# Kernel optimization log

Hardware: AMD Instinct MI355X
Metric: run time of the kernel (lower is better)

The kernel has to match this reference:

```python
import jax, jax.numpy as jnp
import numpy as np

N, H, HD = 512, 8, 128          # n_nodes, n_heads, h feature dim
M0, M1 = 256, 256               # mlp_units
NORM_CONST = 1.0


def setup_inputs() -> dict:
    key = jax.random.key(0)
    ks = jax.random.split(key, 16)
    def w(k, i, o, scale=1.0):
        return jax.random.normal(k, (i, o), jnp.float32) * (scale / np.sqrt(i))
    F = HD + H * H               # h_concat dim = 128 + 64 = 192
    EIN = H + 2 * F              # edge MLP input dim = 8 + 384 = 392
    return {
        "x": jax.random.normal(ks[0], (N, H, 3), jnp.float32),
        "h": jax.random.normal(ks[1], (N, HD), jnp.float32),
        # phi_e: MLP([256,256], silu, activate_final=True)
        "We0": w(ks[2], EIN, M0), "be0": jnp.zeros((M0,), jnp.float32),
        "We1": w(ks[3], M0, M1), "be1": jnp.zeros((M1,), jnp.float32),
        # phi_inf: Linear(1) + sigmoid
        "Winf": w(ks[4], M1, 1), "binf": jnp.zeros((1,), jnp.float32),
        # phi_x: MLP([256,256], silu, activate_final=True) -> Linear(n_heads) (variance-scaled small init)
        "Wx0": w(ks[5], M1, M0), "bx0": jnp.zeros((M0,), jnp.float32),
        "Wx1": w(ks[6], M0, M1), "bx1": jnp.zeros((M1,), jnp.float32),
        "Wxo": w(ks[7], M1, H, scale=0.03), "bxo": jnp.zeros((H,), jnp.float32),
        # phi_h: MLP([256,256], silu, activate_final=False)... note haiku MLP applies
        # activation between layers; final Linear(h_dim) appended in forward.
        "Wh0": w(ks[8], M1 + HD, M0), "bh0": jnp.zeros((M0,), jnp.float32),
        "Wh1": w(ks[9], M0, M1), "bh1": jnp.zeros((M1,), jnp.float32),
        "Who": w(ks[10], M1, HD), "bho": jnp.zeros((HD,), jnp.float32),
    }


def _forward(x, h, We0, be0, We1, be1, Winf, binf, Wx0, bx0, Wx1, bx1,
             Wxo, bxo, Wh0, bh0, Wh1, bh1, Who, bho):
    n, nh = x.shape[0], x.shape[1]
    silu = jax.nn.silu
    off = 1.0 - jnp.eye(n, dtype=x.dtype)                  # off-diagonal node mask
    # per-node head-pair squared distances -> [N, H*H] (diag naturally 0)
    dh = x[:, :, None, :] - x[:, None, :, :]               # [N,H,H,3]
    sqh = jnp.sum(dh * dh, axis=-1).reshape(n, nh * nh)
    hc = jnp.concatenate([h, sqh], axis=-1)                # [N, F]
    # all-pairs node diffs per head: dn[i,j,h] = x[j,h] - x[i,h]
    dn = x[None] - x[:, None]                              # [N,N,H,3]
    sqn = jnp.sum(dn * dn, axis=-1)                        # [N,N,H]
    F = hc.shape[-1]
    hc_j = jnp.broadcast_to(hc[None], (n, n, F))           # receiver-side: hc[j]
    hc_i = jnp.broadcast_to(hc[:, None], (n, n, F))        # sender-side: hc[i]
    edge_in = jnp.concatenate([sqn, hc_j, hc_i], axis=-1)  # [N,N,H+2F]
    # phi_e (activate_final=True), zero self-edges
    m = silu(silu(edge_in @ We0 + be0) @ We1 + be1) * off[:, :, None]
    # gate + message aggregation
    e = jax.nn.sigmoid(m @ Winf + binf)[..., 0] * off      # [N,N]
    m_i = jnp.einsum('ijd,ij->id', m, e)                   # [N,M1]
    # phi_x multi-head coordinate weights (tanh=False), zero self-edges
    px = (silu(silu(m @ Wx0 + bx0) @ Wx1 + bx1) @ Wxo + bxo) * off[:, :, None]
    # normalize_by_x_norm=True path
    norm = jnp.sqrt(sqn + 1e-8) + NORM_CONST               # [N,N,H]
    ndiff = (dn / norm[..., None]) * off[:, :, None, None]
    shift = jnp.einsum('ijhd,ijh->ihd', ndiff, px) / (n - 1)  # agg='mean'
    x_new = x + shift
    # phi_h with residual
    ph_in = jnp.concatenate([m_i, h], axis=-1)
    h_new = h + silu(silu(ph_in @ Wh0 + bh0) @ Wh1 + bh1) @ Who + bho
    return x_new, h_new


def reference(x, h, We0, be0, We1, be1, Winf, binf, Wx0, bx0, Wx1, bx1,
              Wxo, bxo, Wh0, bh0, Wh1, bh1, Who, bho):
    return _forward(x, h, We0, be0, We1, be1, Winf, binf, Wx0, bx0, Wx1, bx1,
                    Wxo, bxo, Wh0, bh0, Wh1, bh1, Who, bho)
```

## Files before the change

kernel.cpp:

```cpp
#include <hip/hip_runtime.h>
#include <math.h>

#define N_NODES 512
#define NH 8
#define HD 128
#define M 256
#define JTILE 64

typedef __bf16 v8bf __attribute__((ext_vector_type(8)));
typedef float f32x4 __attribute__((ext_vector_type(4)));
typedef unsigned uint2v __attribute__((ext_vector_type(2)));

__device__ __forceinline__ float silu_f(float v) {
  return v * __builtin_amdgcn_rcpf(1.f + __expf(-v));
}
__device__ __forceinline__ float sigmoid_f(float v) {
  return __builtin_amdgcn_rcpf(1.f + __expf(-v));
}
__device__ __forceinline__ unsigned short f2bf(float f) {
  unsigned u = __float_as_uint(f);
  u += 0x7fffu + ((u >> 16) & 1u);
  return (unsigned short)(u >> 16);
}
__device__ __forceinline__ float bf2f_lo(unsigned u) {
  return __uint_as_float(u << 16);
}
__device__ __forceinline__ float bf2f_hi(unsigned u) {
  return __uint_as_float(u & 0xffff0000u);
}
__device__ __forceinline__ unsigned cvt_pk_bf16(float lo, float hi) {
  unsigned r;
  asm("v_cvt_pk_bf16_f32 %0, %1, %2" : "=v"(r) : "v"(lo), "v"(hi));
  return r;
}

__global__ __launch_bounds__(256) void k_pre(
    const float* __restrict__ x, const float* __restrict__ h,
    const float* __restrict__ We0, const float* __restrict__ be0,
    const float* __restrict__ We1, const float* __restrict__ Wx0,
    const float* __restrict__ Wx1, const float* __restrict__ Wxo,
    unsigned short* __restrict__ wsB,
    float* __restrict__ P, float* __restrict__ Q,
    float* __restrict__ mi, float* __restrict__ shift)
{
  const int t = threadIdx.x;
  if (blockIdx.x < 816) {
    const int gid = blockIdx.x * 256 + t;
    if (gid >= 208896) return;
    float val;
    int dst;
    if (gid < 196608) {
      const int layer = gid >> 16, e = gid & 65535;
      const int k = e >> 8, n = e & 255;
      const float* W = (layer == 0) ? We1 : (layer == 1) ? Wx0 : Wx1;
      val = W[e];
      const int kt = k >> 5, w = k & 31, quad = w >> 3, j = w & 7;
      const int nt = n >> 4, lnib = n & 15;
      dst = layer * 65536 + ((kt * 16 + nt) * 64 + quad * 16 + lnib) * 8 + j;
    } else if (gid < 198656) {
      const int e = gid - 196608;
      val = Wxo[e];
      const int k = e >> 3, col = e & 7;
      const int kt = k >> 5, w = k & 31, quad = w >> 3, j = w & 7;
      dst = 196608 + (kt * 64 + quad * 16 + col) * 8 + j;
    } else if (gid < 200704) {
      const int e = gid - 198656;
      val = 0.f;
      const int k = e >> 3, col = e & 7;
      const int kt = k >> 5, w = k & 31, quad = w >> 3, j = w & 7;
      dst = 196608 + (kt * 64 + quad * 16 + col + 8) * 8 + j;
    } else if (gid < 202752) {
      const int e = gid - 200704;
      val = We0[e];
      const int j = e >> 8, n = e & 255, nt = n >> 4, lnib = n & 15;
      dst = 200704 + (nt * 64 + lnib) * 8 + j;
    } else {
      const int e = gid - 202752;
      val = 0.f;
      const int q = 1 + (e >> 11), rem = e & 2047;
      const int j = rem & 7, lnib = (rem >> 3) & 15, nt = rem >> 7;
      dst = 200704 + (nt * 64 + q * 16 + lnib) * 8 + j;
    }
    wsB[dst] = f2bf(val);
    return;
  }
  const int i = blockIdx.x - 816;
  __shared__ float s_x[24];
  __shared__ float s_hc[192];
  mi[i * M + t] = 0.f;
  if (t < 24) { shift[i * 24 + t] = 0.f; s_x[t] = x[i * 24 + t]; }
  __syncthreads();
  if (t < HD) {
    s_hc[t] = h[i * HD + t];
  } else if (t < 192) {
    const int p = t - HD, a = p >> 3, b = p & 7;
    float s = 0.f;
#pragma unroll
    for (int d = 0; d < 3; ++d) {
      const float dx = s_x[a * 3 + d] - s_x[b * 3 + d];
      s = fmaf(dx, dx, s);
    }
    s_hc[t] = s;
  }
  __syncthreads();
  float p = 0.f, q = 0.f;
  for (int k = 0; k < 192; ++k) {
    const float hv = s_hc[k];
    p = fmaf(hv, We0[(8 + k) * M + t], p);
    q = fmaf(hv, We0[(200 + k) * M + t], q);
  }
  P[i * M + t] = p;
  Q[i * M + t] = q + be0[t];
}

__global__ __launch_bounds__(256, 3) void k_edge(
    const float* __restrict__ x,
    const float* __restrict__ P, const float* __restrict__ Q,
    const float* __restrict__ be1,
    const float* __restrict__ Winf, const float* __restrict__ binf,
    const float* __restrict__ bx0, const float* __restrict__ bx1,
    const float* __restrict__ bxo,
    const unsigned short* __restrict__ wsB,
    float* __restrict__ mi_acc, float* __restrict__ shift_acc)
{
  const int i  = blockIdx.x;
  const int j0 = blockIdx.y * JTILE;
  const int t  = threadIdx.x;
  const int lane = t & 63, wq = t >> 6;
  const int lnib = lane & 15, quad = lane >> 4;
  const int cb = wq * 64;

  __shared__ __align__(16) unsigned short a_act[32 * 512];
  __shared__ __align__(16) float s_sqn[JTILE][8];
  __shared__ __align__(16) unsigned short s_sqnb[JTILE][8];
  __shared__ float s_red[JTILE][4];
  __shared__ float s_e[JTILE];

  f32x4 acc[4][4];

  auto store_frag = [&](int ct, int et, unsigned w0, unsigned w1) {
    const int tile = et * 8 + 2 * wq + (ct >> 1);
    const int qp   = (ct & 1) * 2 + (quad >> 1);
    const int sidx = (tile * 64 + qp * 16 + lnib) * 8 + (quad & 1) * 4;
    *(uint2v*)&a_act[sidx] = (uint2v){w0, w1};
  };

  auto run_gemm = [&](const unsigned short* __restrict__ Bg) {
#pragma unroll
    for (int kt = 0; kt < 8; ++kt) {
      v8bf wf[4], af[4];
#pragma unroll
      for (int ct = 0; ct < 4; ++ct)
        wf[ct] = *(const v8bf*)&Bg[((kt * 16 + wq * 4 + ct) * 64 + lane) * 8];
#pragma unroll
      for (int et = 0; et < 4; ++et)
        af[et] = *(const v8bf*)&a_act[((et * 8 + kt) * 64 + lane) * 8];
#pragma unroll
      for (int ct = 0; ct < 4; ++ct)
#pragma unroll
        for (int et = 0; et < 4; ++et)
          acc[ct][et] = __builtin_amdgcn_mfma_f32_16x16x32_bf16(wf[ct], af[et], acc[ct][et], 0, 0, 0);
    }
  };

#pragma unroll
  for (int kk = 0; kk < 2; ++kk) {
    const int idx = kk * 256 + t;
    const int r = idx >> 3, hh = idx & 7;
    const int j = j0 + r;
    float s = 0.f;
#pragma unroll
    for (int d = 0; d < 3; ++d) {
      const float dx = x[j * 24 + hh * 3 + d] - x[i * 24 + hh * 3 + d];
      s = fmaf(dx, dx, s);
    }
    s_sqn[r][hh] = s;
    s_sqnb[r][hh] = f2bf(s);
  }
  const float binf0 = binf[0];
  __syncthreads();

  {
#pragma unroll
    for (int ct = 0; ct < 4; ++ct)
#pragma unroll
      for (int et = 0; et < 4; ++et)
        acc[ct][et] = *(const f32x4*)&P[(j0 + et * 16 + lnib) * M + cb + ct * 16 + quad * 4];
    const unsigned short* W0 = wsB + 200704;
    v8bf wf[4], af[4];
#pragma unroll
    for (int ct = 0; ct < 4; ++ct)
      wf[ct] = *(const v8bf*)&W0[((wq * 4 + ct) * 64 + lane) * 8];
#pragma unroll
    for (int et = 0; et < 4; ++et)
      af[et] = *(const v8bf*)&s_sqnb[et * 16 + lnib][0];
#pragma unroll
    for (int ct = 0; ct < 4; ++ct)
#pragma unroll
      for (int et = 0; et < 4; ++et)
        acc[ct][et] = __builtin_amdgcn_mfma_f32_16x16x32_bf16(wf[ct], af[et], acc[ct][et], 0, 0, 0);
#pragma unroll
    for (int ct = 0; ct < 4; ++ct) {
      const f32x4 qv = *(const f32x4*)&Q[i * M + cb + ct * 16 + quad * 4];
#pragma unroll
      for (int et = 0; et < 4; ++et) {
        const unsigned w0 = cvt_pk_bf16(silu_f(acc[ct][et][0] + qv[0]),
                                        silu_f(acc[ct][et][1] + qv[1]));
        const unsigned w1 = cvt_pk_bf16(silu_f(acc[ct][et][2] + qv[2]),
                                        silu_f(acc[ct][et][3] + qv[3]));
        store_frag(ct, et, w0, w1);
      }
    }
  }

#pragma unroll
  for (int ct = 0; ct < 4; ++ct) {
    const f32x4 b = *(const f32x4*)&be1[cb + ct * 16 + quad * 4];
#pragma unroll
    for (int et = 0; et < 4; ++et) acc[ct][et] = b;
  }
  __syncthreads();
  run_gemm(wsB);
  __syncthreads();

  unsigned mw[4][4][2];
  {
    float ge[4] = {0.f, 0.f, 0.f, 0.f};
#pragma unroll
    for (int ct = 0; ct < 4; ++ct) {
      const f32x4 wv = *(const f32x4*)&Winf[cb + ct * 16 + quad * 4];
#pragma unroll
      for (int et = 0; et < 4; ++et) {
        const int row = et * 16 + lnib;
        const bool dz = (j0 + row == i);
        const float v0 = dz ? 0.f : silu_f(acc[ct][et][0]);
        const float v1 = dz ? 0.f : silu_f(acc[ct][et][1]);
        const float v2 = dz ? 0.f : silu_f(acc[ct][et][2]);
        const float v3 = dz ? 0.f : silu_f(acc[ct][et][3]);
        ge[et] = fmaf(v0, wv[0], ge[et]);
        ge[et] = fmaf(v1, wv[1], ge[et]);
        ge[et] = fmaf(v2, wv[2], ge[et]);
        ge[et] = fmaf(v3, wv[3], ge[et]);
        const unsigned w0 = cvt_pk_bf16(v0, v1);
        const unsigned w1 = cvt_pk_bf16(v2, v3);
        mw[ct][et][0] = w0; mw[ct][et][1] = w1;
        store_frag(ct, et, w0, w1);
      }
    }
#pragma unroll
    for (int et = 0; et < 4; ++et) {
      float g = ge[et];
      g += __shfl_xor(g, 16);
      g += __shfl_xor(g, 32);
      if (quad == 0) s_red[et * 16 + lnib][wq] = g;
    }
  }
  __syncthreads();
  if (t < JTILE)
    s_e[t] = sigmoid_f(s_red[t][0] + s_red[t][1] + s_red[t][2] + s_red[t][3] + binf0);
  __syncthreads();

  {
    float ev[4];
#pragma unroll
    for (int et = 0; et < 4; ++et) ev[et] = s_e[et * 16 + lnib];
    float s[4][4];
#pragma unroll
    for (int ct = 0; ct < 4; ++ct) {
      s[ct][0] = 0.f; s[ct][1] = 0.f; s[ct][2] = 0.f; s[ct][3] = 0.f;
#pragma unroll
      for (int et = 0; et < 4; ++et) {
        s[ct][0] = fmaf(bf2f_lo(mw[ct][et][0]), ev[et], s[ct][0]);
        s[ct][1] = fmaf(bf2f_hi(mw[ct][et][0]), ev[et], s[ct][1]);
        s[ct][2] = fmaf(bf2f_lo(mw[ct][et][1]), ev[et], s[ct][2]);
        s[ct][3] = fmaf(bf2f_hi(mw[ct][et][1]), ev[et], s[ct][3]);
      }
    }
#pragma unroll
    for (int ct = 0; ct < 4; ++ct)
#pragma unroll
      for (int r = 0; r < 4; ++r) {
        float v = s[ct][r];
        v += __shfl_xor(v, 1);
        v += __shfl_xor(v, 2);
        v += __shfl_xor(v, 4);
        v += __shfl_xor(v, 8);
        s[ct][r] = v;
      }
    if (lnib == 0) {
#pragma unroll
      for (int ct = 0; ct < 4; ++ct)
#pragma unroll
        for (int r = 0; r < 4; ++r)
          atomicAdd(&mi_acc[i * M + cb + ct * 16 + quad * 4 + r], s[ct][r]);
    }
  }

#pragma unroll
  for (int ct = 0; ct < 4; ++ct) {
    const f32x4 b = *(const f32x4*)&bx0[cb + ct * 16 + quad * 4];
#pragma unroll
    for (int et = 0; et < 4; ++et) acc[ct][et] = b;
  }
  run_gemm(wsB + 65536);
  __syncthreads();
#pragma unroll
  for (int ct = 0; ct < 4; ++ct)
#pragma unroll
    for (int et = 0; et < 4; ++et) {
      const unsigned w0 = cvt_pk_bf16(silu_f(acc[ct][et][0]), silu_f(acc[ct][et][1]));
      const unsigned w1 = cvt_pk_bf16(silu_f(acc[ct][et][2]), silu_f(acc[ct][et][3]));
      store_frag(ct, et, w0, w1);
    }

#pragma unroll
  for (int ct = 0; ct < 4; ++ct) {
    const f32x4 b = *(const f32x4*)&bx1[cb + ct * 16 + quad * 4];
#pragma unroll
    for (int et = 0; et < 4; ++et) acc[ct][et] = b;
  }
  __syncthreads();
  run_gemm(wsB + 131072);
  __syncthreads();
#pragma unroll
  for (int ct = 0; ct < 4; ++ct)
#pragma unroll
    for (int et = 0; et < 4; ++et) {
      const unsigned w0 = cvt_pk_bf16(silu_f(acc[ct][et][0]), silu_f(acc[ct][et][1]));
      const unsigned w1 = cvt_pk_bf16(silu_f(acc[ct][et][2]), silu_f(acc[ct][et][3]));
      store_frag(ct, et, w0, w1);
    }
  __syncthreads();

  {
    f32x4 px;
    if (quad < 2) px = *(const f32x4*)&bxo[quad * 4];
    else          px = (f32x4){0.f, 0.f, 0.f, 0.f};
    const unsigned short* Bx = wsB + 196608;
#pragma unroll
    for (int kt = 0; kt < 8; ++kt) {
      const v8bf af = *(const v8bf*)&a_act[((wq * 8 + kt) * 64 + lane) * 8];
      const v8bf wf = *(const v8bf*)&Bx[(kt * 64 + lane) * 8];
      px = __builtin_amdgcn_mfma_f32_16x16x32_bf16(wf, af, px, 0, 0, 0);
    }
    const int e0 = wq * 16;
    const int jg = j0 + e0 + lnib;
    float c0[4], c1[4], c2[4];
#pragma unroll
    for (int r = 0; r < 4; ++r) { c0[r] = 0.f; c1[r] = 0.f; c2[r] = 0.f; }
    if (quad < 2 && jg != i) {
#pragma unroll
      for (int r = 0; r < 4; ++r) {
        const int hh = quad * 4 + r;
        const float sq = s_sqn[e0 + lnib][hh];
        const float f  = px[r] * __builtin_amdgcn_rcpf(sqrtf(sq + 1e-8f) + 1.f);
        c0[r] = (x[jg * 24 + hh * 3 + 0] - x[i * 24 + hh * 3 + 0]) * f;
        c1[r] = (x[jg * 24 + hh * 3 + 1] - x[i * 24 + hh * 3 + 1]) * f;
        c2[r] = (x[jg * 24 + hh * 3 + 2] - x[i * 24 + hh * 3 + 2]) * f;
      }
    }
#pragma unroll
    for (int r = 0; r < 4; ++r) {
#pragma unroll
      for (int s = 1; s <= 8; s <<= 1) {
        c0[r] += __shfl_xor(c0[r], s);
        c1[r] += __shfl_xor(c1[r], s);
        c2[r] += __shfl_xor(c2[r], s);
      }
    }
    if (lnib == 0 && quad < 2) {
#pragma unroll
      for (int r = 0; r < 4; ++r) {
        const int hh = quad * 4 + r;
        atomicAdd(&shift_acc[i * 24 + hh * 3 + 0], c0[r]);
        atomicAdd(&shift_acc[i * 24 + hh * 3 + 1], c1[r]);
        atomicAdd(&shift_acc[i * 24 + hh * 3 + 2], c2[r]);
      }
    }
  }
}

__global__ __launch_bounds__(256) void k_hout(
    const float* __restrict__ x, const float* __restrict__ shift,
    const float* __restrict__ h, const float* __restrict__ mi,
    const float* __restrict__ Wh0, const float* __restrict__ bh0,
    const float* __restrict__ Wh1, const float* __restrict__ bh1,
    const float* __restrict__ Who, const float* __restrict__ bho,
    float* __restrict__ out_x, float* __restrict__ out_h)
{
  const int i = blockIdx.x, t = threadIdx.x;
  __shared__ float s_in[M + HD];
  __shared__ float s_b[M];
  if (t < 24) out_x[i * 24 + t] = x[i * 24 + t] + shift[i * 24 + t] * (1.f / 511.f);
  s_in[t] = mi[i * M + t];
  if (t < HD) s_in[M + t] = h[i * HD + t];
  __syncthreads();
  float acc = bh0[t];
  for (int k = 0; k < M + HD; ++k) acc = fmaf(s_in[k], Wh0[k * M + t], acc);
  s_b[t] = silu_f(acc);
  __syncthreads();
  float acc2 = bh1[t];
  for (int k = 0; k < M; ++k) acc2 = fmaf(s_b[k], Wh1[k * M + t], acc2);
  const float a1v = silu_f(acc2);
  __syncthreads();
  s_in[t] = a1v;
  __syncthreads();
  if (t < HD) {
    float o = bho[t];
    for (int k = 0; k < M; ++k) o = fmaf(s_in[k], Who[k * HD + t], o);
    out_h[i * HD + t] = h[i * HD + t] + o;
  }
}

extern "C" void kernel_launch(void* const* d_in, const int* in_sizes, int n_in,
                              void* d_out, int out_size, void* d_ws, size_t ws_size,
                              hipStream_t stream)
{
  const float* x    = (const float*)d_in[0];
  const float* h    = (const float*)d_in[1];
  const float* We0  = (const float*)d_in[2];
  const float* be0  = (const float*)d_in[3];
  const float* We1  = (const float*)d_in[4];
  const float* be1  = (const float*)d_in[5];
  const float* Winf = (const float*)d_in[6];
  const float* binf = (const float*)d_in[7];
  const float* Wx0  = (const float*)d_in[8];
  const float* bx0  = (const float*)d_in[9];
  const float* Wx1  = (const float*)d_in[10];
  const float* bx1  = (const float*)d_in[11];
  const float* Wxo  = (const float*)d_in[12];
  const float* bxo  = (const float*)d_in[13];
  const float* Wh0  = (const float*)d_in[14];
  const float* bh0  = (const float*)d_in[15];
  const float* Wh1  = (const float*)d_in[16];
  const float* bh1  = (const float*)d_in[17];
  const float* Who  = (const float*)d_in[18];
  const float* bho  = (const float*)d_in[19];

  float* out_x = (float*)d_out;
  float* out_h = out_x + N_NODES * NH * 3;

  float* ws    = (float*)d_ws;
  float* mi    = ws;
  float* shift = ws + 131072;
  float* P     = ws + 143360;
  float* Q     = ws + 274432;
  unsigned short* wsB = (unsigned short*)(ws + 405504);

  k_pre<<<816 + N_NODES, 256, 0, stream>>>(
      x, h, We0, be0, We1, Wx0, Wx1, Wxo, wsB, P, Q, mi, shift);
  k_edge<<<dim3(N_NODES, N_NODES / JTILE), 256, 0, stream>>>(
      x, P, Q, be1, Winf, binf, bx0, bx1, bxo, wsB, mi, shift);
  k_hout<<<N_NODES, 256, 0, stream>>>(
      x, shift, h, mi, Wh0, bh0, Wh1, bh1, Who, bho, out_x, out_h);
}
```

Measured before the change: 285.0 us.

## Split edge kernel columns across 8 waves with 512-thread blocks

The edge kernel now runs 512 threads per block. Each of the 8 waves owns 32 output columns instead of 64, which halves the per-thread accumulator tiles. The register-held bf16 message copy is dropped, and the message aggregation re-reads the fragments from shared memory instead. The aim is fewer registers per thread and more resident waves to hide MFMA and memory latency, at the cost of more LDS reads, an 8-way gate reduction, and idle waves in the final projection stage.

```diff
diff --git a/kernel.cpp b/kernel.cpp
--- a/kernel.cpp
+++ b/kernel.cpp
@@ -113,7 +113,7 @@
   Q[i * M + t] = q + be0[t];
 }
 
-__global__ __launch_bounds__(256, 3) void k_edge(
+__global__ __launch_bounds__(512, 6) void k_edge(
     const float* __restrict__ x,
     const float* __restrict__ P, const float* __restrict__ Q,
     const float* __restrict__ be1,
@@ -128,45 +128,44 @@
   const int t  = threadIdx.x;
   const int lane = t & 63, wq = t >> 6;
   const int lnib = lane & 15, quad = lane >> 4;
-  const int cb = wq * 64;
+  const int cb = wq * 32;
 
   __shared__ __align__(16) unsigned short a_act[32 * 512];
   __shared__ __align__(16) float s_sqn[JTILE][8];
   __shared__ __align__(16) unsigned short s_sqnb[JTILE][8];
-  __shared__ float s_red[JTILE][4];
+  __shared__ float s_red[JTILE][8];
   __shared__ float s_e[JTILE];
 
-  f32x4 acc[4][4];
-
+  f32x4 acc[2][4];
+
+  auto frag_addr = [&](int ct, int et) {
+    return (((et * 8 + wq) * 64) + (ct * 2 + (quad >> 1)) * 16 + lnib) * 8 +
+           (quad & 1) * 4;
+  };
   auto store_frag = [&](int ct, int et, unsigned w0, unsigned w1) {
-    const int tile = et * 8 + 2 * wq + (ct >> 1);
-    const int qp   = (ct & 1) * 2 + (quad >> 1);
-    const int sidx = (tile * 64 + qp * 16 + lnib) * 8 + (quad & 1) * 4;
-    *(uint2v*)&a_act[sidx] = (uint2v){w0, w1};
+    *(uint2v*)&a_act[frag_addr(ct, et)] = (uint2v){w0, w1};
   };
 
   auto run_gemm = [&](const unsigned short* __restrict__ Bg) {
 #pragma unroll
     for (int kt = 0; kt < 8; ++kt) {
-      v8bf wf[4], af[4];
-#pragma unroll
-      for (int ct = 0; ct < 4; ++ct)
-        wf[ct] = *(const v8bf*)&Bg[((kt * 16 + wq * 4 + ct) * 64 + lane) * 8];
+      v8bf wf[2], af[4];
+#pragma unroll
+      for (int ct = 0; ct < 2; ++ct)
+        wf[ct] = *(const v8bf*)&Bg[((kt * 16 + wq * 2 + ct) * 64 + lane) * 8];
 #pragma unroll
       for (int et = 0; et < 4; ++et)
         af[et] = *(const v8bf*)&a_act[((et * 8 + kt) * 64 + lane) * 8];
 #pragma unroll
-      for (int ct = 0; ct < 4; ++ct)
+      for (int ct = 0; ct < 2; ++ct)
 #pragma unroll
         for (int et = 0; et < 4; ++et)
           acc[ct][et] = __builtin_amdgcn_mfma_f32_16x16x32_bf16(wf[ct], af[et], acc[ct][et], 0, 0, 0);
     }
   };
 
-#pragma unroll
-  for (int kk = 0; kk < 2; ++kk) {
-    const int idx = kk * 256 + t;
-    const int r = idx >> 3, hh = idx & 7;
+  {
+    const int r = t >> 3, hh = t & 7;
     const int j = j0 + r;
     float s = 0.f;
 #pragma unroll
@@ -182,25 +181,25 @@
 
   {
 #pragma unroll
-    for (int ct = 0; ct < 4; ++ct)
+    for (int ct = 0; ct < 2; ++ct)
 #pragma unroll
       for (int et = 0; et < 4; ++et)
         acc[ct][et] = *(const f32x4*)&P[(j0 + et * 16 + lnib) * M + cb + ct * 16 + quad * 4];
     const unsigned short* W0 = wsB + 200704;
-    v8bf wf[4], af[4];
-#pragma unroll
-    for (int ct = 0; ct < 4; ++ct)
-      wf[ct] = *(const v8bf*)&W0[((wq * 4 + ct) * 64 + lane) * 8];
+    v8bf wf[2], af[4];
+#pragma unroll
+    for (int ct = 0; ct < 2; ++ct)
+      wf[ct] = *(const v8bf*)&W0[((wq * 2 + ct) * 64 + lane) * 8];
 #pragma unroll
     for (int et = 0; et < 4; ++et)
       af[et] = *(const v8bf*)&s_sqnb[et * 16 + lnib][0];
 #pragma unroll
-    for (int ct = 0; ct < 4; ++ct)
+    for (int ct = 0; ct < 2; ++ct)
 #pragma unroll
       for (int et = 0; et < 4; ++et)
         acc[ct][et] = __builtin_amdgcn_mfma_f32_16x16x32_bf16(wf[ct], af[et], acc[ct][et], 0, 0, 0);
 #pragma unroll
-    for (int ct = 0; ct < 4; ++ct) {
+    for (int ct = 0; ct < 2; ++ct) {
       const f32x4 qv = *(const f32x4*)&Q[i * M + cb + ct * 16 + quad * 4];
 #pragma unroll
       for (int et = 0; et < 4; ++et) {
@@ -214,7 +213,7 @@
   }
 
 #pragma unroll
-  for (int ct = 0; ct < 4; ++ct) {
+  for (int ct = 0; ct < 2; ++ct) {
     const f32x4 b = *(const f32x4*)&be1[cb + ct * 16 + quad * 4];
 #pragma unroll
     for (int et = 0; et < 4; ++et) acc[ct][et] = b;
@@ -223,11 +222,10 @@
   run_gemm(wsB);
   __syncthreads();
 
-  unsigned mw[4][4][2];
   {
     float ge[4] = {0.f, 0.f, 0.f, 0.f};
 #pragma unroll
-    for (int ct = 0; ct < 4; ++ct) {
+    for (int ct = 0; ct < 2; ++ct) {
       const f32x4 wv = *(const f32x4*)&Winf[cb + ct * 16 + quad * 4];
 #pragma unroll
       for (int et = 0; et < 4; ++et) {
@@ -241,10 +239,7 @@
         ge[et] = fmaf(v1, wv[1], ge[et]);
         ge[et] = fmaf(v2, wv[2], ge[et]);
         ge[et] = fmaf(v3, wv[3], ge[et]);
-        const unsigned w0 = cvt_pk_bf16(v0, v1);
-        const unsigned w1 = cvt_pk_bf16(v2, v3);
-        mw[ct][et][0] = w0; mw[ct][et][1] = w1;
-        store_frag(ct, et, w0, w1);
+        store_frag(ct, et, cvt_pk_bf16(v0, v1), cvt_pk_bf16(v2, v3));
       }
     }
 #pragma unroll
@@ -256,28 +251,33 @@
     }
   }
   __syncthreads();
-  if (t < JTILE)
-    s_e[t] = sigmoid_f(s_red[t][0] + s_red[t][1] + s_red[t][2] + s_red[t][3] + binf0);
+  if (t < JTILE) {
+    float g = binf0;
+#pragma unroll
+    for (int w = 0; w < 8; ++w) g += s_red[t][w];
+    s_e[t] = sigmoid_f(g);
+  }
   __syncthreads();
 
   {
     float ev[4];
 #pragma unroll
     for (int et = 0; et < 4; ++et) ev[et] = s_e[et * 16 + lnib];
-    float s[4][4];
-#pragma unroll
-    for (int ct = 0; ct < 4; ++ct) {
+    float s[2][4];
+#pragma unroll
+    for (int ct = 0; ct < 2; ++ct) {
       s[ct][0] = 0.f; s[ct][1] = 0.f; s[ct][2] = 0.f; s[ct][3] = 0.f;
 #pragma unroll
       for (int et = 0; et < 4; ++et) {
-        s[ct][0] = fmaf(bf2f_lo(mw[ct][et][0]), ev[et], s[ct][0]);
-        s[ct][1] = fmaf(bf2f_hi(mw[ct][et][0]), ev[et], s[ct][1]);
-        s[ct][2] = fmaf(bf2f_lo(mw[ct][et][1]), ev[et], s[ct][2]);
-        s[ct][3] = fmaf(bf2f_hi(mw[ct][et][1]), ev[et], s[ct][3]);
-      }
-    }
-#pragma unroll
-    for (int ct = 0; ct < 4; ++ct)
+        const uint2v pw = *(const uint2v*)&a_act[frag_addr(ct, et)];
+        s[ct][0] = fmaf(bf2f_lo(pw[0]), ev[et], s[ct][0]);
+        s[ct][1] = fmaf(bf2f_hi(pw[0]), ev[et], s[ct][1]);
+        s[ct][2] = fmaf(bf2f_lo(pw[1]), ev[et], s[ct][2]);
+        s[ct][3] = fmaf(bf2f_hi(pw[1]), ev[et], s[ct][3]);
+      }
+    }
+#pragma unroll
+    for (int ct = 0; ct < 2; ++ct)
 #pragma unroll
       for (int r = 0; r < 4; ++r) {
         float v = s[ct][r];
@@ -289,7 +289,7 @@
       }
     if (lnib == 0) {
 #pragma unroll
-      for (int ct = 0; ct < 4; ++ct)
+      for (int ct = 0; ct < 2; ++ct)
 #pragma unroll
         for (int r = 0; r < 4; ++r)
           atomicAdd(&mi_acc[i * M + cb + ct * 16 + quad * 4 + r], s[ct][r]);
@@ -297,7 +297,7 @@
   }
 
 #pragma unroll
-  for (int ct = 0; ct < 4; ++ct) {
+  for (int ct = 0; ct < 2; ++ct) {
     const f32x4 b = *(const f32x4*)&bx0[cb + ct * 16 + quad * 4];
 #pragma unroll
     for (int et = 0; et < 4; ++et) acc[ct][et] = b;
@@ -305,7 +305,7 @@
   run_gemm(wsB + 65536);
   __syncthreads();
 #pragma unroll
-  for (int ct = 0; ct < 4; ++ct)
+  for (int ct = 0; ct < 2; ++ct)
 #pragma unroll
     for (int et = 0; et < 4; ++et) {
       const unsigned w0 = cvt_pk_bf16(silu_f(acc[ct][et][0]), silu_f(acc[ct][et][1]));
@@ -314,7 +314,7 @@
     }
 
 #pragma unroll
-  for (int ct = 0; ct < 4; ++ct) {
+  for (int ct = 0; ct < 2; ++ct) {
     const f32x4 b = *(const f32x4*)&bx1[cb + ct * 16 + quad * 4];
 #pragma unroll
     for (int et = 0; et < 4; ++et) acc[ct][et] = b;
@@ -323,7 +323,7 @@
   run_gemm(wsB + 131072);
   __syncthreads();
 #pragma unroll
-  for (int ct = 0; ct < 4; ++ct)
+  for (int ct = 0; ct < 2; ++ct)
 #pragma unroll
     for (int et = 0; et < 4; ++et) {
       const unsigned w0 = cvt_pk_bf16(silu_f(acc[ct][et][0]), silu_f(acc[ct][et][1]));
@@ -332,7 +332,7 @@
     }
   __syncthreads();
 
-  {
+  if (wq < 4) {
     f32x4 px;
     if (quad < 2) px = *(const f32x4*)&bxo[quad * 4];
     else          px = (f32x4){0.f, 0.f, 0.f, 0.f};
@@ -449,7 +449,7 @@
 
   k_pre<<<816 + N_NODES, 256, 0, stream>>>(
       x, h, We0, be0, We1, Wx0, Wx1, Wxo, wsB, P, Q, mi, shift);
-  k_edge<<<dim3(N_NODES, N_NODES / JTILE), 256, 0, stream>>>(
+  k_edge<<<dim3(N_NODES, N_NODES / JTILE), 512, 0, stream>>>(
       x, P, Q, be1, Winf, binf, bx0, bx1, bxo, wsB, mi, shift);
   k_hout<<<N_NODES, 256, 0, stream>>>(
       x, shift, h, mi, Wh0, bh0, Wh1, bh1, Who, bho, out_x, out_h);
```

Result: slower. 317.1 us (+11.3%).
